# Optimization experiments

Measured on AMD Instinct MI355X. Metric: run time of the kernel, lower is better.

Reference implementation:

```python
import jax, jax.numpy as jnp
import numpy as np

N_PTS0 = 32   # sample points per line
N_PTS1 = 8    # after maxpool1d (kernel/stride = 4)
DIM_LOI = 128
DIM_FC = 1024
TOPK = 300
HW = 128
NLINES = 20000
NLAB = 3


def setup_inputs() -> dict:
    key = jax.random.key(0)
    ks = jax.random.split(key, 10)
    jloc = jax.random.uniform(ks[0], (1, HW, HW), dtype=jnp.float32)
    joff = jax.random.uniform(ks[1], (2, HW, HW), dtype=jnp.float32)
    loi_features = jax.random.normal(ks[2], (DIM_LOI, HW, HW), dtype=jnp.float32)
    edge_idx = jax.random.randint(ks[3], (NLINES, 2), 0, TOPK, dtype=jnp.int32)
    W1 = jax.random.normal(ks[4], (DIM_LOI * N_PTS1, DIM_FC), dtype=jnp.float32) * 0.02
    b1 = jnp.zeros((DIM_FC,), jnp.float32)
    W2 = jax.random.normal(ks[5], (DIM_FC, DIM_FC), dtype=jnp.float32) * 0.02
    b2 = jnp.zeros((DIM_FC,), jnp.float32)
    W3 = jax.random.normal(ks[6], (DIM_FC, NLAB), dtype=jnp.float32) * 0.02
    b3 = jnp.zeros((NLAB,), jnp.float32)
    return {"jloc": jloc, "joff": joff, "loi_features": loi_features,
            "edge_idx": edge_idx, "W1": W1, "b1": b1, "W2": W2, "b2": b2,
            "W3": W3, "b3": b3}


def reference(jloc, joff, loi_features, edge_idx, W1, b1, W2, b2, W3, b3):
    C, h, w = loi_features.shape
    # --- NMS: 3x3 max_pool2d, keep only local maxima ---
    ap = jax.lax.reduce_window(jloc, -jnp.inf, jax.lax.max,
                               (1, 3, 3), (1, 1, 1), 'SAME')
    jloc_nms = jloc * (jloc == ap).astype(jloc.dtype)
    # --- top-k junction decoding (joff_pred = sigmoid(joff) - 0.5) ---
    joff_pred = jax.nn.sigmoid(joff) - 0.5
    scores, idx = jax.lax.top_k(jloc_nms.reshape(-1), TOPK)
    joff_flat = joff_pred.reshape(2, -1)
    y = (idx // w).astype(jnp.float32) + joff_flat[1][idx] + 0.5
    x = (idx % w).astype(jnp.float32) + joff_flat[0][idx] + 0.5
    juncs = jnp.stack((x, y), axis=1)                       # [K, 2]
    # --- lines from junction pairs (lines_adjusted) ---
    lines = jnp.concatenate((juncs[edge_idx[:, 0]], juncs[edge_idx[:, 1]]), axis=1)  # [N, 4]
    # --- LOI pooling: bilinear sampling along each line ---
    tspan = jnp.linspace(0.0, 1.0, N_PTS0)                  # [P]
    U, V = lines[:, :2], lines[:, 2:]
    pts = U[:, :, None] * tspan + V[:, :, None] * (1.0 - tspan) - 0.5  # [N, 2, P]
    pts = pts.transpose(0, 2, 1).reshape(-1, 2)             # [N*P, 2]
    px, py = pts[:, 0], pts[:, 1]
    px0 = jnp.clip(jnp.floor(px), 0, w - 1)
    py0 = jnp.clip(jnp.floor(py), 0, h - 1)
    px1 = jnp.clip(px0 + 1, 0, w - 1)
    py1 = jnp.clip(py0 + 1, 0, h - 1)
    px0l, py0l = px0.astype(jnp.int32), py0.astype(jnp.int32)
    px1l, py1l = px1.astype(jnp.int32), py1.astype(jnp.int32)
    xp = (loi_features[:, py0l, px0l] * (py1 - py) * (px1 - px)
          + loi_features[:, py1l, px0l] * (py - py0) * (px1 - px)
          + loi_features[:, py0l, px1l] * (py1 - py) * (px - px0)
          + loi_features[:, py1l, px1l] * (py - py0) * (px - px0))  # [C, N*P]
    xp = xp.reshape(C, -1, N_PTS0).transpose(1, 0, 2)        # [N, C, P]
    k = N_PTS0 // N_PTS1
    xp = xp.reshape(xp.shape[0], C, N_PTS1, k).max(axis=-1)  # maxpool1d
    feats = xp.reshape(xp.shape[0], C * N_PTS1)              # [N, C*n_pts1]
    # --- fc2 MLP head ---
    h1 = jax.nn.relu(feats @ W1 + b1)
    h2 = jax.nn.relu(h1 @ W2 + b2)
    line_logits = h2 @ W3 + b3
    return line_logits
```

## Files before the change

### kernel.cpp

```cpp
#include <hip/hip_runtime.h>
#include <cmath>


typedef _Float16 f16;
typedef _Float16 f16x2 __attribute__((ext_vector_type(2)));
typedef _Float16 f16x8 __attribute__((ext_vector_type(8)));
typedef float f32x4 __attribute__((ext_vector_type(4)));

#define HWD 128
#define NPIX 16384
#define TOPK_N 300
#define NLINES 20000
#define MPAD 20096
#define KDIM 1024
#define NDIM 1024
#define MAXCAND 4096

#define G2L(gp, lp) __builtin_amdgcn_global_load_lds( \
    (const __attribute__((address_space(1))) void*)(gp), \
    (__attribute__((address_space(3))) void*)(lp), 16, 0, 0)

__global__ __launch_bounds__(256) void preproc_kernel(
    const float* __restrict__ loi, f16* __restrict__ loiT,
    const float* __restrict__ W1, f16* __restrict__ W1T,
    const float* __restrict__ W2, f16* __restrict__ W2T,
    const float* __restrict__ jloc, unsigned long long* __restrict__ cand,
    int* __restrict__ count, float* __restrict__ out, int out_n)
{
    const int bid = blockIdx.x;
    const int tid = threadIdx.x;
    if (bid < 128) {
        __shared__ f16 t[128 * 130];
        const int y = bid;
        #pragma unroll 4
        for (int it = 0; it < 64; ++it) {
            int idx = it * 256 + tid;
            int c = idx >> 7, x = idx & 127;
            t[x * 130 + c] = (f16)loi[c * NPIX + y * HWD + x];
        }
        __syncthreads();
        #pragma unroll
        for (int it = 0; it < 8; ++it) {
            int j = it * 256 + tid;
            int x = j >> 4, cc = (j & 15) * 8;
            f16x8 v;
            #pragma unroll
            for (int u = 0; u < 8; ++u) v[u] = t[x * 130 + cc + u];
            *(f16x8*)(loiT + (y * HWD + x) * HWD + cc) = v;
        }
    } else if (bid < 640) {
        const int b = bid - 128;
        const float* W = (b < 256) ? W1 : W2;
        f16* Wt = (b < 256) ? W1T : W2T;
        const int bb = b & 255;
        __shared__ f16 t[64 * 66];
        const int k0 = (bb >> 4) * 64;
        const int n0 = (bb & 15) * 64;
        #pragma unroll 4
        for (int it = 0; it < 16; ++it) {
            int i = it * 256 + tid;
            int r = i >> 6, c = i & 63;
            t[c * 66 + r] = (f16)W[(size_t)(k0 + r) * NDIM + n0 + c];
        }
        __syncthreads();
        #pragma unroll
        for (int it = 0; it < 2; ++it) {
            int j = it * 256 + tid;
            int nr = j >> 3, kc = (j & 7) * 8;
            f16x8 v;
            #pragma unroll
            for (int u = 0; u < 8; ++u) v[u] = t[nr * 66 + kc + u];
            const int kk = k0 + kc;
            *(f16x8*)(Wt + ((size_t)(kk >> 5) * NDIM + (n0 + nr)) * 32 + (kk & 31)) = v;
        }
    } else if (bid < 704) {
        const int p = (bid - 640) * 256 + tid;
        const int y = p >> 7, x = p & 127;
        const float c = jloc[p];
        float m = c;
        for (int dy = -1; dy <= 1; ++dy) {
            int yy = y + dy;
            if (yy < 0 || yy >= HWD) continue;
            for (int dx = -1; dx <= 1; ++dx) {
                int xx = x + dx;
                if (xx < 0 || xx >= HWD) continue;
                m = fmaxf(m, jloc[yy * HWD + xx]);
            }
        }
        if (c == m && c > 0.0f) {
            int pos = atomicAdd(count, 1);
            if (pos < MAXCAND) {
                unsigned int ub = __float_as_uint(c);
                cand[pos] = ((unsigned long long)ub << 32) |
                            (unsigned long long)(0xFFFFFFFFu - (unsigned int)p);
            }
        }
    } else {
        const int base = (bid - 704) * 1024 + tid * 4;
        #pragma unroll
        for (int u = 0; u < 4; ++u)
            if (base + u < out_n) out[base + u] = 0.f;
    }
}

__global__ __launch_bounds__(256) void rank_junc_kernel(
    const unsigned long long* __restrict__ cand, const int* __restrict__ count,
    const float* __restrict__ joff, float* __restrict__ juncs )
{
    __shared__ unsigned long long keys[MAXCAND];
    const int n = min(*count, MAXCAND);
    const int t = blockIdx.x * 256 + threadIdx.x;
    for (int i = threadIdx.x; i < n; i += 256)
        keys[i] = cand[i];
    __syncthreads();
    if (t >= n) return;
    const unsigned long long key = keys[t];
    int rank = 0;
    int j = 0;
    for (; j + 4 <= n; j += 4) {
        rank += (keys[j]     > key);
        rank += (keys[j + 1] > key);
        rank += (keys[j + 2] > key);
        rank += (keys[j + 3] > key);
    }
    for (; j < n; ++j) rank += (keys[j] > key);
    if (rank < TOPK_N) {
        unsigned int p = 0xFFFFFFFFu - (unsigned int)(key & 0xFFFFFFFFull);
        float sx = 1.0f / (1.0f + expf(-joff[p]));
        float sy = 1.0f / (1.0f + expf(-joff[NPIX + p]));
        juncs[2 * rank + 0] = (float)(p & 127) + sx;
        juncs[2 * rank + 1] = (float)(p >> 7) + sy;
    }
}

__global__ __launch_bounds__(256) void sample_kernel(
    const f16* __restrict__ loiT, const float* __restrict__ juncs,
    const int* __restrict__ edge_idx, f16* __restrict__ feats)
{
    const int wv = threadIdx.x >> 6;
    const int l = blockIdx.x * 4 + wv;
    const int lane = threadIdx.x & 63;

    __shared__ int   soff[4][32][4];
    __shared__ float swt[4][32][4];

    if (lane < 32) {
        const int e0 = edge_idx[2 * l], e1 = edge_idx[2 * l + 1];
        const float ux = juncs[2 * e0], uy = juncs[2 * e0 + 1];
        const float vx = juncs[2 * e1], vy = juncs[2 * e1 + 1];
        const int j = lane;
        const float t = (float)j * (1.0f / 31.0f);
        const float px = ux * t + vx * (1.0f - t) - 0.5f;
        const float py = uy * t + vy * (1.0f - t) - 0.5f;
        float fx0 = fminf(fmaxf(floorf(px), 0.0f), 127.0f);
        float fy0 = fminf(fmaxf(floorf(py), 0.0f), 127.0f);
        float fx1 = fminf(fx0 + 1.0f, 127.0f);
        float fy1 = fminf(fy0 + 1.0f, 127.0f);
        int ix0 = (int)fx0, iy0 = (int)fy0, ix1 = (int)fx1, iy1 = (int)fy1;
        soff[wv][j][0] = (iy0 * HWD + ix0) * HWD;
        soff[wv][j][1] = (iy1 * HWD + ix0) * HWD;
        soff[wv][j][2] = (iy0 * HWD + ix1) * HWD;
        soff[wv][j][3] = (iy1 * HWD + ix1) * HWD;
        swt[wv][j][0] = (fy1 - py) * (fx1 - px);
        swt[wv][j][1] = (py - fy0) * (fx1 - px);
        swt[wv][j][2] = (fy1 - py) * (px - fx0);
        swt[wv][j][3] = (py - fy0) * (px - fx0);
    }
    __syncthreads();

    const int c2 = lane * 2;
    f16x8 o0, o1;
    #pragma unroll
    for (int p = 0; p < 8; ++p) {
        float m0 = -INFINITY, m1 = -INFINITY;
        #pragma unroll
        for (int jj = 0; jj < 4; ++jj) {
            const int j = p * 4 + jj;
            const int b00 = soff[wv][j][0], b10 = soff[wv][j][1];
            const int b01 = soff[wv][j][2], b11 = soff[wv][j][3];
            const float w00 = swt[wv][j][0], w10 = swt[wv][j][1];
            const float w01 = swt[wv][j][2], w11 = swt[wv][j][3];
            f16x2 v00 = *(const f16x2*)(loiT + b00 + c2);
            f16x2 v10 = *(const f16x2*)(loiT + b10 + c2);
            f16x2 v01 = *(const f16x2*)(loiT + b01 + c2);
            f16x2 v11 = *(const f16x2*)(loiT + b11 + c2);
            float s0 = (float)v00.x * w00 + (float)v10.x * w10 +
                       (float)v01.x * w01 + (float)v11.x * w11;
            float s1 = (float)v00.y * w00 + (float)v10.y * w10 +
                       (float)v01.y * w01 + (float)v11.y * w11;
            m0 = fmaxf(m0, s0);
            m1 = fmaxf(m1, s1);
        }
        o0[p] = (f16)m0;
        o1[p] = (f16)m1;
    }
    f16* dst = feats + ((size_t)(lane >> 1) * MPAD + l) * 32 + (lane & 1) * 16;
    *(f16x8*)(dst) = o0;
    *(f16x8*)(dst + 8) = o1;
}

__global__ __launch_bounds__(256, 2) void gemm_bias_relu_kernel(
    const f16* __restrict__ A, const f16* __restrict__ Bt,
    const float* __restrict__ bias, f16* __restrict__ C,
    const float* __restrict__ W3, const float* __restrict__ b3,
    float* __restrict__ out, int K, int head)
{
    const int tid = threadIdx.x;
    const int wave = tid >> 6, lane = tid & 63;
    const int wm = wave >> 1, wn = wave & 1;
    const int m0 = blockIdx.x * 128;
    const int n0 = blockIdx.y * 128;
    const int N = NDIM;

    __shared__ f16 sA0[128 * 32];
    __shared__ f16 sA1[128 * 32];
    __shared__ f16 sB0[128 * 32];
    __shared__ f16 sB1[128 * 32];

    f32x4 acc[4][4];
    #pragma unroll
    for (int mi = 0; mi < 4; ++mi)
        #pragma unroll
        for (int ni = 0; ni < 4; ++ni)
            acc[mi][ni] = (f32x4){0.f, 0.f, 0.f, 0.f};

    const size_t strideA = (size_t)MPAD * 32;
    const size_t strideB = (size_t)NDIM * 32;
    const f16* gA = A + (size_t)m0 * 32 + wave * 512 + lane * 8;
    const f16* gB = Bt + (size_t)n0 * 32 + wave * 512 + lane * 8;
    const int so0 = wave * 512;
    const int so1 = (wave + 4) * 512;

    const int col16 = lane & 15;
    const int kq = (lane >> 4) * 8;

    const int NC = K >> 5;
    for (int c0 = 0; c0 < NC; c0 += 2) {
        const f16* a0 = gA + (size_t)c0 * strideA;
        const f16* a1 = a0 + strideA;
        const f16* b0 = gB + (size_t)c0 * strideB;
        const f16* b1 = b0 + strideB;
        __syncthreads();
        G2L(a0, sA0 + so0);
        G2L(a0 + 2048, sA0 + so1);
        G2L(b0, sB0 + so0);
        G2L(b0 + 2048, sB0 + so1);
        G2L(a1, sA1 + so0);
        G2L(a1 + 2048, sA1 + so1);
        G2L(b1, sB1 + so0);
        G2L(b1 + 2048, sB1 + so1);
        __builtin_amdgcn_s_waitcnt(0x0f70);
        __syncthreads();

        {
            f16x8 af[4], bf[4];
            #pragma unroll
            for (int i = 0; i < 4; ++i) {
                af[i] = *(const f16x8*)(sA0 + (wm * 64 + i * 16 + col16) * 32 + kq);
                bf[i] = *(const f16x8*)(sB0 + (wn * 64 + i * 16 + col16) * 32 + kq);
            }
            #pragma unroll
            for (int mi = 0; mi < 4; ++mi)
                #pragma unroll
                for (int ni = 0; ni < 4; ++ni)
                    acc[mi][ni] = __builtin_amdgcn_mfma_f32_16x16x32_f16(
                        af[mi], bf[ni], acc[mi][ni], 0, 0, 0);
        }
        {
            f16x8 af[4], bf[4];
            #pragma unroll
            for (int i = 0; i < 4; ++i) {
                af[i] = *(const f16x8*)(sA1 + (wm * 64 + i * 16 + col16) * 32 + kq);
                bf[i] = *(const f16x8*)(sB1 + (wn * 64 + i * 16 + col16) * 32 + kq);
            }
            #pragma unroll
            for (int mi = 0; mi < 4; ++mi)
                #pragma unroll
                for (int ni = 0; ni < 4; ++ni)
                    acc[mi][ni] = __builtin_amdgcn_mfma_f32_16x16x32_f16(
                        af[mi], bf[ni], acc[mi][ni], 0, 0, 0);
        }
    }

    const int quad = lane >> 4;
    if (!head) {
        #pragma unroll
        for (int ni = 0; ni < 4; ++ni) {
            const int n = n0 + wn * 64 + ni * 16 + col16;
            const float b = bias[n];
            const size_t cb = ((size_t)(n >> 5) * MPAD) * 32 + (n & 31);
            #pragma unroll
            for (int mi = 0; mi < 4; ++mi) {
                #pragma unroll
                for (int r = 0; r < 4; ++r) {
                    const int m = m0 + wm * 64 + mi * 16 + quad * 4 + r;
                    float v = fmaxf(acc[mi][ni][r] + b, 0.f);
                    C[cb + (size_t)m * 32] = (f16)v;
                }
            }
        }
    } else {
        float bb[4], w3c[4][3];
        #pragma unroll
        for (int ni = 0; ni < 4; ++ni) {
            const int n = n0 + wn * 64 + ni * 16 + col16;
            bb[ni] = bias[n];
            #pragma unroll
            for (int jj = 0; jj < 3; ++jj) w3c[ni][jj] = W3[n * 3 + jj];
        }
        const bool addb3 = (blockIdx.y == 0 && wn == 0);
        #pragma unroll
        for (int mi = 0; mi < 4; ++mi) {
            #pragma unroll
            for (int r = 0; r < 4; ++r) {
                float s0 = 0.f, s1 = 0.f, s2 = 0.f;
                #pragma unroll
                for (int ni = 0; ni < 4; ++ni) {
                    float v = fmaxf(acc[mi][ni][r] + bb[ni], 0.f);
                    s0 += v * w3c[ni][0];
                    s1 += v * w3c[ni][1];
                    s2 += v * w3c[ni][2];
                }
                #pragma unroll
                for (int mask = 1; mask <= 8; mask <<= 1) {
                    s0 += __shfl_xor(s0, mask);
                    s1 += __shfl_xor(s1, mask);
                    s2 += __shfl_xor(s2, mask);
                }
                if (col16 == 0) {
                    const int m = m0 + wm * 64 + mi * 16 + quad * 4 + r;
                    if (m < NLINES) {
                        atomicAdd(&out[m * 3 + 0], s0 + (addb3 ? b3[0] : 0.f));
                        atomicAdd(&out[m * 3 + 1], s1 + (addb3 ? b3[1] : 0.f));
                        atomicAdd(&out[m * 3 + 2], s2 + (addb3 ? b3[2] : 0.f));
                    }
                }
            }
        }
    }
}

extern "C" void kernel_launch(void* const* d_in, const int* in_sizes, int n_in,
                              void* d_out, int out_size, void* d_ws, size_t ws_size,
                              hipStream_t stream)
{
    const float* jloc = (const float*)d_in[0];
    const float* joff = (const float*)d_in[1];
    const float* loi  = (const float*)d_in[2];
    const int*   eidx = (const int*)d_in[3];
    const float* W1   = (const float*)d_in[4];
    const float* b1   = (const float*)d_in[5];
    const float* W2   = (const float*)d_in[6];
    const float* b2   = (const float*)d_in[7];
    const float* W3   = (const float*)d_in[8];
    const float* b3   = (const float*)d_in[9];
    float* out = (float*)d_out;

    char* ws = (char*)d_ws;
    f16*   loiT  = (f16*)(ws);
    f16*   W1T   = (f16*)(ws + ((size_t)4 << 20));
    f16*   W2T   = (f16*)(ws + ((size_t)6 << 20));
    float* juncs = (float*)(ws + ((size_t)8 << 20));
    int*   count = (int*)(ws + ((size_t)8 << 20) + 4096);
    unsigned long long* cand =
        (unsigned long long*)(ws + ((size_t)8 << 20) + 8192);
    f16*   feats = (f16*)(ws + ((size_t)9 << 20));
    f16*   h1    = (f16*)(ws + ((size_t)51 << 20));

    hipMemsetAsync(count, 0, sizeof(int), stream);
    preproc_kernel<<<dim3(764), dim3(256), 0, stream>>>(
        loi, loiT, W1, W1T, W2, W2T, jloc, cand, count, out, out_size);
    rank_junc_kernel<<<dim3(MAXCAND / 256), dim3(256), 0, stream>>>(
        cand, count, joff, juncs);
    sample_kernel<<<dim3(NLINES / 4), dim3(256), 0, stream>>>(loiT, juncs, eidx, feats);
    gemm_bias_relu_kernel<<<dim3(MPAD / 128, NDIM / 128), dim3(256), 0, stream>>>(
        feats, W1T, b1, h1, nullptr, nullptr, nullptr, KDIM, 0);
    gemm_bias_relu_kernel<<<dim3(MPAD / 128, NDIM / 128), dim3(256), 0, stream>>>(
        h1, W2T, b2, nullptr, W3, b3, out, KDIM, 1);
}
```

Measured before the change: 310.9 us.

## Sort lines by start junction for sampling locality and enlarge GEMM M-tile to 256

Adds a single-block counting-sort kernel that orders lines by their first junction index, and the sampler processes lines in that order to improve cache locality of bilinear gathers. The GEMM is changed to 512-thread blocks with a 256-row M tile (8 waves), which halves B-tile reloads per output and pads M to a multiple of 256. The single-block sort adds a serial launch, and the new GEMM launch bounds may change occupancy and register pressure. The GEMM epilogue (hidden) must match the new 8-wave layout for correctness.

```diff
diff --git a/kernel.cpp b/kernel.cpp
--- a/kernel.cpp
+++ b/kernel.cpp
@@ -11,7 +11,7 @@
 #define NPIX 16384
 #define TOPK_N 300
 #define NLINES 20000
-#define MPAD 20096
+#define MPAD 20224
 #define KDIM 1024
 #define NDIM 1024
 #define MAXCAND 4096
@@ -100,6 +100,28 @@
         #pragma unroll
         for (int u = 0; u < 4; ++u)
             if (base + u < out_n) out[base + u] = 0.f;
+    }
+}
+
+__global__ __launch_bounds__(1024) void sort_lines_kernel(
+    const int* __restrict__ edge_idx, int* __restrict__ order)
+{
+    __shared__ int hist[TOPK_N];
+    __shared__ int base[TOPK_N];
+    const int tid = threadIdx.x;
+    for (int i = tid; i < TOPK_N; i += 1024) hist[i] = 0;
+    __syncthreads();
+    for (int i = tid; i < NLINES; i += 1024)
+        atomicAdd(&hist[edge_idx[2 * i]], 1);
+    __syncthreads();
+    if (tid == 0) {
+        int acc = 0;
+        for (int b = 0; b < TOPK_N; ++b) { base[b] = acc; acc += hist[b]; }
+    }
+    __syncthreads();
+    for (int i = tid; i < NLINES; i += 1024) {
+        int pos = atomicAdd(&base[edge_idx[2 * i]], 1);
+        order[pos] = i;
     }
 }
 
@@ -135,10 +157,11 @@
 
 __global__ __launch_bounds__(256) void sample_kernel(
     const f16* __restrict__ loiT, const float* __restrict__ juncs,
-    const int* __restrict__ edge_idx, f16* __restrict__ feats)
+    const int* __restrict__ edge_idx, const int* __restrict__ order,
+    f16* __restrict__ feats)
 {
     const int wv = threadIdx.x >> 6;
-    const int l = blockIdx.x * 4 + wv;
+    const int l = order[blockIdx.x * 4 + wv];
     const int lane = threadIdx.x & 63;
 
     __shared__ int   soff[4][32][4];
@@ -199,7 +222,7 @@
     *(f16x8*)(dst + 8) = o1;
 }
 
-__global__ __launch_bounds__(256, 2) void gemm_bias_relu_kernel(
+__global__ __launch_bounds__(512) void gemm_bias_relu_kernel(
     const f16* __restrict__ A, const f16* __restrict__ Bt,
     const float* __restrict__ bias, f16* __restrict__ C,
     const float* __restrict__ W3, const float* __restrict__ b3,
@@ -208,12 +231,11 @@
     const int tid = threadIdx.x;
     const int wave = tid >> 6, lane = tid & 63;
     const int wm = wave >> 1, wn = wave & 1;
-    const int m0 = blockIdx.x * 128;
+    const int m0 = blockIdx.x * 256;
     const int n0 = blockIdx.y * 128;
-    const int N = NDIM;
-
-    __shared__ f16 sA0[128 * 32];
-    __shared__ f16 sA1[128 * 32];
+
+    __shared__ f16 sA0[256 * 32];
+    __shared__ f16 sA1[256 * 32];
     __shared__ f16 sB0[128 * 32];
     __shared__ f16 sB1[128 * 32];
 
@@ -226,10 +248,11 @@
 
     const size_t strideA = (size_t)MPAD * 32;
     const size_t strideB = (size_t)NDIM * 32;
-    const f16* gA = A + (size_t)m0 * 32 + wave * 512 + lane * 8;
-    const f16* gB = Bt + (size_t)n0 * 32 + wave * 512 + lane * 8;
-    const int so0 = wave * 512;
-    const int so1 = (wave + 4) * 512;
+    const f16* gA = A + (size_t)m0 * 32 + lane * 8;
+    const f16* gB = Bt + (size_t)n0 * 32 + lane * 8;
+    const int sa0 = wave * 512;
+    const int sa1 = (wave + 8) * 512;
+    const int sb = wave * 512;
 
     const int col16 = lane & 15;
     const int kq = (lane >> 4) * 8;
@@ -241,14 +264,12 @@
         const f16* b0 = gB + (size_t)c0 * strideB;
         const f16* b1 = b0 + strideB;
         __syncthreads();
-        G2L(a0, sA0 + so0);
-        G2L(a0 + 2048, sA0 + so1);
-        G2L(b0, sB0 + so0);
-        G2L(b0 + 2048, sB0 + so1);
-        G2L(a1, sA1 + so0);
-        G2L(a1 + 2048, sA1 + so1);
-        G2L(b1, sB1 + so0);
-        G2L(b1 + 2048, sB1 + so1);
+        G2L(a0 + sa0, sA0 + sa0);
+        G2L(a0 + sa1, sA0 + sa1);
+        G2L(b0 + sb, sB0 + sb);
+        G2L(a1 + sa0, sA1 + sa0);
+        G2L(a1 + sa1, sA1 + sa1);
+        G2L(b1 + sb, sB1 + sb);
         __builtin_amdgcn_s_waitcnt(0x0f70);
         __syncthreads();
 
@@ -364,17 +385,20 @@
     int*   count = (int*)(ws + ((size_t)8 << 20) + 4096);
     unsigned long long* cand =
         (unsigned long long*)(ws + ((size_t)8 << 20) + 8192);
+    int*   order = (int*)(ws + ((size_t)8 << 20) + 65536);
     f16*   feats = (f16*)(ws + ((size_t)9 << 20));
     f16*   h1    = (f16*)(ws + ((size_t)51 << 20));
 
     hipMemsetAsync(count, 0, sizeof(int), stream);
     preproc_kernel<<<dim3(764), dim3(256), 0, stream>>>(
         loi, loiT, W1, W1T, W2, W2T, jloc, cand, count, out, out_size);
+    sort_lines_kernel<<<dim3(1), dim3(1024), 0, stream>>>(eidx, order);
     rank_junc_kernel<<<dim3(MAXCAND / 256), dim3(256), 0, stream>>>(
         cand, count, joff, juncs);
-    sample_kernel<<<dim3(NLINES / 4), dim3(256), 0, stream>>>(loiT, juncs, eidx, feats);
-    gemm_bias_relu_kernel<<<dim3(MPAD / 128, NDIM / 128), dim3(256), 0, stream>>>(
+    sample_kernel<<<dim3(NLINES / 4), dim3(256), 0, stream>>>(
+        loiT, juncs, eidx, order, feats);
+    gemm_bias_relu_kernel<<<dim3(MPAD / 256, NDIM / 128), dim3(512), 0, stream>>>(
         feats, W1T, b1, h1, nullptr, nullptr, nullptr, KDIM, 0);
-    gemm_bias_relu_kernel<<<dim3(MPAD / 128, NDIM / 128), dim3(256), 0, stream>>>(
+    gemm_bias_relu_kernel<<<dim3(MPAD / 256, NDIM / 128), dim3(512), 0, stream>>>(
         h1, W2T, b2, nullptr, W3, b3, out, KDIM, 1);
 }
```

Measured after the change: 360.4 us. +15.9%, slower.
